# Kernel tuning notes

Hardware: AMD Instinct MI355X
Metric: run time of the kernel (lower is better)

## Reference

```python
import jax, jax.numpy as jnp
import numpy as np
from jax import lax

DIM = 8        # per-head dim
HEADS = 32     # inp // dim
EPS = 1e-15    # linear-attention eps
BN_EPS = 1e-5  # torch BatchNorm2d default eps


def _conv(x, w, groups=1, pad=0):
    return lax.conv_general_dilated(
        x, w, window_strides=(1, 1), padding=[(pad, pad), (pad, pad)],
        feature_group_count=groups,
        dimension_numbers=('NCHW', 'OIHW', 'NCHW'))


def setup_inputs() -> dict:
    key = jax.random.key(0)
    ks = jax.random.split(key, 9)
    B, C, H, W = 8, 256, 64, 64
    td = HEADS * DIM  # 256
    x = jax.random.normal(ks[0], (B, C, H, W), jnp.float32)
    w_qkv = jax.random.normal(ks[1], (3 * td, C, 1, 1), jnp.float32) * 0.05
    w_dw = jax.random.normal(ks[2], (3 * td, 1, 5, 5), jnp.float32) * 0.05
    w_pw = jax.random.normal(ks[3], (3 * td, (3 * td) // (3 * HEADS), 1, 1), jnp.float32) * 0.05
    w_proj = jax.random.normal(ks[4], (C, 2 * td, 1, 1), jnp.float32) * 0.05
    bn_gamma = 1.0 + 0.1 * jax.random.normal(ks[5], (C,), jnp.float32)
    bn_beta = 0.1 * jax.random.normal(ks[6], (C,), jnp.float32)
    bn_mean = 0.1 * jax.random.normal(ks[7], (C,), jnp.float32)
    bn_var = jnp.ones((C,), jnp.float32)
    return dict(x=x, w_qkv=w_qkv, w_dw=w_dw, w_pw=w_pw, w_proj=w_proj,
                bn_gamma=bn_gamma, bn_beta=bn_beta, bn_mean=bn_mean, bn_var=bn_var)


def reference(x, w_qkv, w_dw, w_pw, w_proj, bn_gamma, bn_beta, bn_mean, bn_var):
    B, _, H, W = x.shape
    # qkv: 1x1 conv, no bias/norm/act
    qkv = _conv(x, w_qkv)                                   # (B, 3*td, H, W)
    # aggreg branch: depthwise 5x5 then grouped 1x1 (groups = 3*heads)
    agg = _conv(qkv, w_dw, groups=w_dw.shape[0], pad=2)
    agg = _conv(agg, w_pw, groups=3 * HEADS)
    ms = jnp.concatenate([qkv, agg], axis=1)                # (B, 2*3*td, H, W)
    # relu linear attention
    G = ms.shape[1] // (3 * DIM)                            # 2*heads = 64
    t = ms.reshape(B, G, 3 * DIM, H * W).transpose(0, 1, 3, 2)  # (B, G, N, 3d)
    q = jax.nn.relu(t[..., :DIM])
    k = jax.nn.relu(t[..., DIM:2 * DIM])
    v = t[..., 2 * DIM:]
    v = jnp.pad(v, ((0, 0), (0, 0), (0, 0), (0, 1)), constant_values=1.0)  # ones trick
    kv = jnp.einsum('bgnd,bgne->bgde', k, v)                # (B, G, d, d+1)
    out = jnp.einsum('bgnd,bgde->bgne', q, kv)              # (B, G, N, d+1)
    out = out[..., :-1] / (out[..., -1:] + EPS)
    out = out.transpose(0, 1, 3, 2).reshape(B, G * DIM, H, W)  # (B, 2*td, H, W)
    # proj: 1x1 conv + BatchNorm2d (eval mode), no act
    out = _conv(out, w_proj)
    inv = jax.lax.rsqrt(bn_var + BN_EPS)
    out = (out - bn_mean[:, None, None]) * (inv * bn_gamma)[:, None, None] + bn_beta[:, None, None]
    return out
```

## Files before the change

### kernel.cpp

```cpp
#include <hip/hip_runtime.h>

typedef __bf16 bf16;
typedef __bf16 bf16x4 __attribute__((ext_vector_type(4)));
typedef __bf16 bf16x8 __attribute__((ext_vector_type(8)));
typedef float f32x4 __attribute__((ext_vector_type(4)));

#define NPIX 4096

__global__ __launch_bounds__(256) void split_x(
    const float* __restrict__ x,
    bf16* __restrict__ xTh, bf16* __restrict__ xTm, bf16* __restrict__ xTl)
{
    const int pix = blockIdx.x * 256 + threadIdx.x;
    const int k0  = blockIdx.y * 32;
    const int b   = blockIdx.z;

    const float* __restrict__ src = x + ((size_t)b * 256 + k0) * NPIX + pix;
    float v[32];
#pragma unroll
    for (int kk = 0; kk < 32; ++kk) v[kk] = src[(size_t)kk * NPIX];

    const size_t drow = ((size_t)b * NPIX + pix) * 256 + k0;
#pragma unroll
    for (int c = 0; c < 4; ++c) {
        bf16x8 vh, vm, vl;
#pragma unroll
        for (int j = 0; j < 8; ++j) {
            float val = v[c * 8 + j];
            bf16 h = (bf16)val; float r  = val - (float)h;
            bf16 m = (bf16)r;   float r2 = r - (float)m;
            vh[j] = h; vm[j] = m; vl[j] = (bf16)r2;
        }
        *(bf16x8*)(xTh + drow + c * 8) = vh;
        *(bf16x8*)(xTm + drow + c * 8) = vm;
        *(bf16x8*)(xTl + drow + c * 8) = vl;
    }
}

__global__ __launch_bounds__(256, 2) void qkv_mfma(
    const float* __restrict__ A,
    const bf16* __restrict__ xTh,
    const bf16* __restrict__ xTm,
    const bf16* __restrict__ xTl,
    float* __restrict__ C)
{
    __shared__ bf16 As[3][128][40];

    const int tid  = threadIdx.x;
    const int lane = tid & 63;
    const int wv   = tid >> 6;
    const int col  = lane & 15;
    const int quad = lane >> 4;
    const int wm   = (wv >> 1) * 64;
    const int wn   = (wv & 1) * 64;
    const int n0   = blockIdx.x * 128;
    const int m0   = blockIdx.y * 128;
    const int b    = blockIdx.z;

    const int arow = tid >> 1;
    const int akc  = (tid & 1) * 16;

    const size_t xoff = ((size_t)b * NPIX + n0 + wn) * 256;

    f32x4 acc[4][4] = {};

    float av[16];
    {
        const float* ap = A + (size_t)(m0 + arow) * 256 + akc;
        *(float4*)&av[0]  = *(const float4*)(ap);
        *(float4*)&av[4]  = *(const float4*)(ap + 4);
        *(float4*)&av[8]  = *(const float4*)(ap + 8);
        *(float4*)&av[12] = *(const float4*)(ap + 12);
    }

    for (int k0 = 0; k0 < 256; k0 += 32) {
        __syncthreads();

#pragma unroll
        for (int c = 0; c < 4; ++c) {
            bf16x4 vh, vm, vl;
#pragma unroll
            for (int j = 0; j < 4; ++j) {
                float val = av[c * 4 + j];
                bf16 h = (bf16)val; float r  = val - (float)h;
                bf16 m = (bf16)r;   float r2 = r - (float)m;
                vh[j] = h; vm[j] = m; vl[j] = (bf16)r2;
            }
            *(bf16x4*)&As[0][arow][akc + c * 4] = vh;
            *(bf16x4*)&As[1][arow][akc + c * 4] = vm;
            *(bf16x4*)&As[2][arow][akc + c * 4] = vl;
        }

        if (k0 + 32 < 256) {
            const float* ap = A + (size_t)(m0 + arow) * 256 + k0 + 32 + akc;
            *(float4*)&av[0]  = *(const float4*)(ap);
            *(float4*)&av[4]  = *(const float4*)(ap + 4);
            *(float4*)&av[8]  = *(const float4*)(ap + 8);
            *(float4*)&av[12] = *(const float4*)(ap + 12);
        }

        __syncthreads();

        bf16x8 bh[4], bm[4], bl[4];
#pragma unroll
        for (int t = 0; t < 4; ++t) {
            const size_t brow = xoff + (size_t)(t * 16 + col) * 256 + k0 + quad * 8;
            bh[t] = *(const bf16x8*)(xTh + brow);
            bm[t] = *(const bf16x8*)(xTm + brow);
            bl[t] = *(const bf16x8*)(xTl + brow);
        }
        bf16x8 af[4][3];
#pragma unroll
        for (int s = 0; s < 4; ++s)
#pragma unroll
            for (int p = 0; p < 3; ++p)
                af[s][p] = *(const bf16x8*)&As[p][wm + s * 16 + col][quad * 8];

#pragma unroll
        for (int t = 0; t < 4; ++t)
#pragma unroll
            for (int s = 0; s < 4; ++s)
                acc[s][t] = __builtin_amdgcn_mfma_f32_16x16x32_bf16(af[s][2], bh[t], acc[s][t], 0, 0, 0);
#pragma unroll
        for (int t = 0; t < 4; ++t)
#pragma unroll
            for (int s = 0; s < 4; ++s)
                acc[s][t] = __builtin_amdgcn_mfma_f32_16x16x32_bf16(af[s][0], bl[t], acc[s][t], 0, 0, 0);
#pragma unroll
        for (int t = 0; t < 4; ++t)
#pragma unroll
            for (int s = 0; s < 4; ++s)
                acc[s][t] = __builtin_amdgcn_mfma_f32_16x16x32_bf16(af[s][1], bm[t], acc[s][t], 0, 0, 0);
#pragma unroll
        for (int t = 0; t < 4; ++t)
#pragma unroll
            for (int s = 0; s < 4; ++s)
                acc[s][t] = __builtin_amdgcn_mfma_f32_16x16x32_bf16(af[s][1], bh[t], acc[s][t], 0, 0, 0);
#pragma unroll
        for (int t = 0; t < 4; ++t)
#pragma unroll
            for (int s = 0; s < 4; ++s)
                acc[s][t] = __builtin_amdgcn_mfma_f32_16x16x32_bf16(af[s][0], bm[t], acc[s][t], 0, 0, 0);
#pragma unroll
        for (int t = 0; t < 4; ++t)
#pragma unroll
            for (int s = 0; s < 4; ++s)
                acc[s][t] = __builtin_amdgcn_mfma_f32_16x16x32_bf16(af[s][0], bh[t], acc[s][t], 0, 0, 0);
    }

    float* __restrict__ Cp = C + (size_t)b * 768 * NPIX;
#pragma unroll
    for (int s = 0; s < 4; ++s)
#pragma unroll
        for (int t = 0; t < 4; ++t)
#pragma unroll
            for (int r = 0; r < 4; ++r) {
                const int m = m0 + wm + s * 16 + quad * 4 + r;
                const int n = n0 + wn + t * 16 + col;
                Cp[(size_t)m * NPIX + n] = acc[s][t][r];
            }
}

__global__ __launch_bounds__(256) void dwpw(
    const float* __restrict__ qkv,
    const float* __restrict__ w_dw,
    const float* __restrict__ w_pw,
    float* __restrict__ agg)
{
    __shared__ float sm[8][20][72];

    const int tid = threadIdx.x;
    const int y0  = blockIdx.x * 16;
    const int p   = blockIdx.y;
    const int b   = blockIdx.z;

    const float* __restrict__ src = qkv + ((size_t)b * 768 + 8 * p) * NPIX;

#pragma unroll
    for (int it = 0; it < 10; ++it) {
        int idx = tid + it * 256;
        int c  = idx / 320;
        int r  = idx % 320;
        int sy = r >> 4;
        int x4 = (r & 15) * 4;
        int gy = y0 + sy - 2;
        float4 v = {0.f, 0.f, 0.f, 0.f};
        if ((unsigned)gy < 64u)
            v = *(const float4*)(src + (size_t)c * NPIX + gy * 64 + x4);
        *(float4*)&sm[c][sy][4 + x4] = v;
    }
    if (tid < 160) {
        int c = tid / 20, sy = tid % 20;
        sm[c][sy][2] = 0.f; sm[c][sy][3] = 0.f;
        sm[c][sy][68] = 0.f; sm[c][sy][69] = 0.f;
    }
    __syncthreads();

    const int ty = tid >> 4;
    const int x0 = (tid & 15) * 4;

    float d[8][4];
#pragma unroll
    for (int c = 0; c < 8; ++c) {
        float a0 = 0.f, a1 = 0.f, a2 = 0.f, a3 = 0.f;
        const float* __restrict__ wc = w_dw + (size_t)(8 * p + c) * 25;
#pragma unroll
        for (int ky = 0; ky < 5; ++ky) {
            float r[12];
            *(float4*)&r[0] = *(const float4*)&sm[c][ty + ky][x0];
            *(float4*)&r[4] = *(const float4*)&sm[c][ty + ky][x0 + 4];
            *(float4*)&r[8] = *(const float4*)&sm[c][ty + ky][x0 + 8];
#pragma unroll
            for (int kx = 0; kx < 5; ++kx) {
                const float wv = wc[ky * 5 + kx];
                a0 = fmaf(wv, r[2 + 0 + kx], a0);
                a1 = fmaf(wv, r[2 + 1 + kx], a1);
                a2 = fmaf(wv, r[2 + 2 + kx], a2);
                a3 = fmaf(wv, r[2 + 3 + kx], a3);
            }
        }
        d[c][0] = a0; d[c][1] = a1; d[c][2] = a2; d[c][3] = a3;
    }

    float* __restrict__ dst = agg + ((size_t)b * 768 + 8 * p) * NPIX + (y0 + ty) * 64 + x0;
#pragma unroll
    for (int o = 0; o < 8; ++o) {
        const float* __restrict__ wo = w_pw + (size_t)(8 * p + o) * 8;
        float4 s = {0.f, 0.f, 0.f, 0.f};
#pragma unroll
        for (int i = 0; i < 8; ++i) {
            const float wv = wo[i];
            s.x = fmaf(wv, d[i][0], s.x);
            s.y = fmaf(wv, d[i][1], s.y);
            s.z = fmaf(wv, d[i][2], s.z);
            s.w = fmaf(wv, d[i][3], s.w);
        }
        *(float4*)(dst + (size_t)o * NPIX) = s;
    }
}

__global__ __launch_bounds__(256) void kv_reduce(
    const float* __restrict__ qkv, const float* __restrict__ agg,
    float* __restrict__ kvb)
{
    const int g = blockIdx.x, b = blockIdx.y;
    const float* __restrict__ src = (g < 32) ? qkv : agg;
    const float* __restrict__ base = src + ((size_t)b * 768 + 24 * (g & 31)) * NPIX;

    float acc[72];
#pragma unroll
    for (int i = 0; i < 72; ++i) acc[i] = 0.0f;

    for (int i4 = threadIdx.x; i4 < NPIX / 4; i4 += 256) {
        float4 kf[8], vf[8];
#pragma unroll
        for (int d = 0; d < 8; ++d) {
            float4 t = ((const float4*)(base + (size_t)(8 + d) * NPIX))[i4];
            kf[d].x = fmaxf(0.0f, t.x); kf[d].y = fmaxf(0.0f, t.y);
            kf[d].z = fmaxf(0.0f, t.z); kf[d].w = fmaxf(0.0f, t.w);
        }
#pragma unroll
        for (int e = 0; e < 8; ++e)
            vf[e] = ((const float4*)(base + (size_t)(16 + e) * NPIX))[i4];
#pragma unroll
        for (int d = 0; d < 8; ++d) {
#pragma unroll
            for (int e = 0; e < 8; ++e)
                acc[d * 9 + e] += kf[d].x * vf[e].x + kf[d].y * vf[e].y +
                                  kf[d].z * vf[e].z + kf[d].w * vf[e].w;
            acc[d * 9 + 8] += kf[d].x + kf[d].y + kf[d].z + kf[d].w;
        }
    }

    const int lane = threadIdx.x & 63;
    const int wv   = threadIdx.x >> 6;
#pragma unroll
    for (int i = 0; i < 72; ++i) {
        float v = acc[i];
        v += __shfl_xor(v, 32, 64);
        v += __shfl_xor(v, 16, 64);
        v += __shfl_xor(v, 8, 64);
        v += __shfl_xor(v, 4, 64);
        v += __shfl_xor(v, 2, 64);
        v += __shfl_xor(v, 1, 64);
        acc[i] = v;
    }
    __shared__ float red[4][72];
    if (lane == 0) {
#pragma unroll
        for (int i = 0; i < 72; ++i) red[wv][i] = acc[i];
    }
    __syncthreads();
    if (threadIdx.x < 72)
        kvb[((size_t)b * 64 + g) * 72 + threadIdx.x] =
            red[0][threadIdx.x] + red[1][threadIdx.x] +
            red[2][threadIdx.x] + red[3][threadIdx.x];
}

__global__ __launch_bounds__(256) void attn_fused(
    const float* __restrict__ qkv, const float* __restrict__ agg,
    const float* __restrict__ kvb,
    bf16* __restrict__ attTh, bf16* __restrict__ attTm)
{
    const int b   = blockIdx.y;
    const int n0  = blockIdx.x * 32;
    const int tid = threadIdx.x;
    const int p   = tid & 31;
    const int c   = tid >> 5;

    __shared__ float kvs[64 * 72];
    for (int i = tid; i < 64 * 72; i += 256) kvs[i] = kvb[(size_t)b * 64 * 72 + i];
    __syncthreads();

    const int n = n0 + p;
    const size_t orow = ((size_t)b * NPIX + n) * 512;

#pragma unroll
    for (int gi = 0; gi < 8; ++gi) {
        const int g = c * 8 + gi;
        const float* __restrict__ src = (g < 32) ? qkv : agg;
        const float* __restrict__ base = src + ((size_t)b * 768 + 24 * (g & 31)) * NPIX + n;

        float q[8];
#pragma unroll
        for (int d = 0; d < 8; ++d) q[d] = fmaxf(0.0f, base[(size_t)d * NPIX]);

        const float* kv = &kvs[g * 72];
        float den = 1e-15f;
#pragma unroll
        for (int d = 0; d < 8; ++d) den = fmaf(q[d], kv[d * 9 + 8], den);
        float inv = 1.0f / den;
#pragma unroll
        for (int d = 0; d < 8; ++d) q[d] *= inv;

        bf16x8 vh, vm;
#pragma unroll
        for (int e = 0; e < 8; ++e) {
            float o = 0.0f;
#pragma unroll
            for (int d = 0; d < 8; ++d) o = fmaf(q[d], kv[d * 9 + e], o);
            bf16 h = (bf16)o;
            vh[e] = h;
            vm[e] = (bf16)(o - (float)h);
        }
        *(bf16x8*)(attTh + orow + g * 8) = vh;
        *(bf16x8*)(attTm + orow + g * 8) = vm;
    }
}

__global__ __launch_bounds__(256, 2) void proj_mfma(
    const float* __restrict__ A,
    const bf16* __restrict__ Bh,
    const bf16* __restrict__ Bm,
    float* __restrict__ C,
    const float* __restrict__ bn_g, const float* __restrict__ bn_b,
    const float* __restrict__ bn_m, const float* __restrict__ bn_v)
{
    __shared__ bf16 As[2][128][40];

    const int tid  = threadIdx.x;
    const int lane = tid & 63;
    const int wv   = tid >> 6;
    const int col  = lane & 15;
    const int quad = lane >> 4;
    const int wm   = (wv >> 1) * 64;
    const int wn   = (wv & 1) * 64;
    const int n0   = blockIdx.x * 128;
    const int m0   = blockIdx.y * 128;
    const int b    = blockIdx.z;

    const int arow = tid >> 1;
    const int akc  = (tid & 1) * 16;

    const size_t boff = ((size_t)b * NPIX + n0 + wn) * 512;

    f32x4 acc[4][4] = {};

    float av[16];
    {
        const float* ap = A + (size_t)(m0 + arow) * 512 + akc;
        *(float4*)&av[0]  = *(const float4*)(ap);
        *(float4*)&av[4]  = *(const float4*)(ap + 4);
        *(float4*)&av[8]  = *(const float4*)(ap + 8);
        *(float4*)&av[12] = *(const float4*)(ap + 12);
    }

    for (int k0 = 0; k0 < 512; k0 += 32) {
        __syncthreads();

#pragma unroll
        for (int c = 0; c < 4; ++c) {
            bf16x4 vh, vm;
#pragma unroll
            for (int j = 0; j < 4; ++j) {
                float val = av[c * 4 + j];
                bf16 h = (bf16)val;
                vh[j] = h; vm[j] = (bf16)(val - (float)h);
            }
            *(bf16x4*)&As[0][arow][akc + c * 4] = vh;
            *(bf16x4*)&As[1][arow][akc + c * 4] = vm;
        }

        if (k0 + 32 < 512) {
            const float* ap = A + (size_t)(m0 + arow) * 512 + k0 + 32 + akc;
            *(float4*)&av[0]  = *(const float4*)(ap);
            *(float4*)&av[4]  = *(const float4*)(ap + 4);
            *(float4*)&av[8]  = *(const float4*)(ap + 8);
            *(float4*)&av[12] = *(const float4*)(ap + 12);
        }

        __syncthreads();

        bf16x8 bh[4], bm2[4];
#pragma unroll
        for (int t = 0; t < 4; ++t) {
            const size_t brow = boff + (size_t)(t * 16 + col) * 512 + k0 + quad * 8;
            bh[t]  = *(const bf16x8*)(Bh + brow);
            bm2[t] = *(const bf16x8*)(Bm + brow);
        }
        bf16x8 af[4][2];
#pragma unroll
        for (int s = 0; s < 4; ++s) {
            af[s][0] = *(const bf16x8*)&As[0][wm + s * 16 + col][quad * 8];
            af[s][1] = *(const bf16x8*)&As[1][wm + s * 16 + col][quad * 8];
        }

#pragma unroll
        for (int t = 0; t < 4; ++t)
#pragma unroll
            for (int s = 0; s < 4; ++s)
                acc[s][t] = __builtin_amdgcn_mfma_f32_16x16x32_bf16(af[s][1], bh[t], acc[s][t], 0, 0, 0);
#pragma unroll
        for (int t = 0; t < 4; ++t)
#pragma unroll
            for (int s = 0; s < 4; ++s)
                acc[s][t] = __builtin_amdgcn_mfma_f32_16x16x32_bf16(af[s][0], bm2[t], acc[s][t], 0, 0, 0);
#pragma unroll
        for (int t = 0; t < 4; ++t)
#pragma unroll
            for (int s = 0; s < 4; ++s)
                acc[s][t] = __builtin_amdgcn_mfma_f32_16x16x32_bf16(af[s][0], bh[t], acc[s][t], 0, 0, 0);
    }

    float* __restrict__ Cp = C + (size_t)b * 256 * NPIX;
#pragma unroll
    for (int s = 0; s < 4; ++s) {
#pragma unroll
        for (int r = 0; r < 4; ++r) {
            const int m = m0 + wm + s * 16 + quad * 4 + r;
            const float sc  = (1.0f / sqrtf(bn_v[m] + 1e-5f)) * bn_g[m];
            const float off = bn_b[m] - bn_m[m] * sc;
#pragma unroll
            for (int t = 0; t < 4; ++t) {
                const int n = n0 + wn + t * 16 + col;
                Cp[(size_t)m * NPIX + n] = acc[s][t][r] * sc + off;
            }
        }
    }
}

extern "C" void kernel_launch(void* const* d_in, const int* in_sizes, int n_in,
                              void* d_out, int out_size, void* d_ws, size_t ws_size,
                              hipStream_t stream) {
    const float* x      = (const float*)d_in[0];
    const float* w_qkv  = (const float*)d_in[1];
    const float* w_dw   = (const float*)d_in[2];
    const float* w_pw   = (const float*)d_in[3];
    const float* w_proj = (const float*)d_in[4];
    const float* bn_g   = (const float*)d_in[5];
    const float* bn_b   = (const float*)d_in[6];
    const float* bn_m   = (const float*)d_in[7];
    const float* bn_v   = (const float*)d_in[8];
    float* out = (float*)d_out;

    char* ws = (char*)d_ws;
    float* qkv  = (float*)ws;
    float* agg  = (float*)(ws + 100663296ull);
    char*  r3   = ws + 201326592ull;
    bf16*  xTh  = (bf16*)r3;
    bf16*  xTm  = (bf16*)(r3 + 16777216ull);
    bf16*  xTl  = (bf16*)(r3 + 33554432ull);
    bf16*  attTh = (bf16*)r3;
    bf16*  attTm = (bf16*)(r3 + 33554432ull);
    float* kvb  = (float*)d_out;

    split_x<<<dim3(16, 8, 8), dim3(256), 0, stream>>>(x, xTh, xTm, xTl);

    qkv_mfma<<<dim3(32, 6, 8), dim3(256), 0, stream>>>(w_qkv, xTh, xTm, xTl, qkv);

    dwpw<<<dim3(4, 96, 8), dim3(256), 0, stream>>>(qkv, w_dw, w_pw, agg);

    kv_reduce<<<dim3(64, 8), dim3(256), 0, stream>>>(qkv, agg, kvb);

    attn_fused<<<dim3(128, 8), dim3(256), 0, stream>>>(qkv, agg, kvb, attTh, attTm);

    proj_mfma<<<dim3(32, 2, 8), dim3(256), 0, stream>>>(
        w_proj, attTh, attTm, out, bn_g, bn_b, bn_m, bn_v);
}
```

Measured before the change: 431.0 us.

## Pre-split GEMM weights to bf16 and double-buffer A tiles via global_load_lds

Adds small kernels that split the qkv and proj weights into bf16 hi/mid/lo parts once per call, so the GEMM blocks no longer convert fp32 weights in registers on every tile. The A operand is now staged with direct global-to-LDS loads into a double-buffered shared tile, and the next tile's load is issued before the MFMAs run, which drops one barrier per k-step. The change adds two kernel launches and some workspace, and uses unpadded LDS rows that may cause bank conflicts. The vmcnt(0) wait also covers the B register loads.

```diff
diff --git a/kernel.cpp b/kernel.cpp
--- a/kernel.cpp
+++ b/kernel.cpp
@@ -37,14 +37,34 @@
     }
 }
 
+__global__ __launch_bounds__(256) void split_w3(
+    const float* __restrict__ w,
+    bf16* __restrict__ h, bf16* __restrict__ m, bf16* __restrict__ l)
+{
+    const int i = blockIdx.x * 256 + threadIdx.x;
+    const float v = w[i];
+    const bf16 a = (bf16)v;  const float r1 = v - (float)a;
+    const bf16 c = (bf16)r1;
+    h[i] = a; m[i] = c; l[i] = (bf16)(r1 - (float)c);
+}
+
+__global__ __launch_bounds__(256) void split_w2(
+    const float* __restrict__ w, bf16* __restrict__ h, bf16* __restrict__ m)
+{
+    const int i = blockIdx.x * 256 + threadIdx.x;
+    const float v = w[i];
+    const bf16 a = (bf16)v;
+    h[i] = a; m[i] = (bf16)(v - (float)a);
+}
+
 __global__ __launch_bounds__(256, 2) void qkv_mfma(
-    const float* __restrict__ A,
-    const bf16* __restrict__ xTh,
-    const bf16* __restrict__ xTm,
+    const bf16* __restrict__ Ah, const bf16* __restrict__ Am,
+    const bf16* __restrict__ Al,
+    const bf16* __restrict__ xTh, const bf16* __restrict__ xTm,
     const bf16* __restrict__ xTl,
     float* __restrict__ C)
 {
-    __shared__ bf16 As[3][128][40];
+    __shared__ __align__(16) bf16 As[2][3][128][32];
 
     const int tid  = threadIdx.x;
     const int lane = tid & 63;
@@ -57,64 +77,63 @@
     const int m0   = blockIdx.y * 128;
     const int b    = blockIdx.z;
 
-    const int arow = tid >> 1;
-    const int akc  = (tid & 1) * 16;
-
     const size_t xoff = ((size_t)b * NPIX + n0 + wn) * 256;
 
+    const int srow = wv * 16 + (lane >> 2);
+    const int schk = (lane & 3) * 8;
+
+    const bf16* AP[3] = {Ah, Am, Al};
+
+    auto stage = [&](int buf, int kk) {
+#pragma unroll
+        for (int p = 0; p < 3; ++p)
+#pragma unroll
+            for (int hh = 0; hh < 2; ++hh) {
+                const bf16* gp = AP[p] + (size_t)(m0 + hh * 64 + srow) * 256 + kk + schk;
+                __builtin_amdgcn_global_load_lds(
+                    (const __attribute__((address_space(1))) void*)gp,
+                    (__attribute__((address_space(3))) void*)&As[buf][p][hh * 64 + wv * 16][0],
+                    16, 0, 0);
+            }
+    };
+
     f32x4 acc[4][4] = {};
 
-    float av[16];
-    {
-        const float* ap = A + (size_t)(m0 + arow) * 256 + akc;
-        *(float4*)&av[0]  = *(const float4*)(ap);
-        *(float4*)&av[4]  = *(const float4*)(ap + 4);
-        *(float4*)&av[8]  = *(const float4*)(ap + 8);
-        *(float4*)&av[12] = *(const float4*)(ap + 12);
-    }
-
+    stage(0, 0);
+
+#pragma unroll
     for (int k0 = 0; k0 < 256; k0 += 32) {
-        __syncthreads();
-
-#pragma unroll
-        for (int c = 0; c < 4; ++c) {
-            bf16x4 vh, vm, vl;
-#pragma unroll
-            for (int j = 0; j < 4; ++j) {
-                float val = av[c * 4 + j];
-                bf16 h = (bf16)val; float r  = val - (float)h;
-                bf16 m = (bf16)r;   float r2 = r - (float)m;
-                vh[j] = h; vm[j] = m; vl[j] = (bf16)r2;
-            }
-            *(bf16x4*)&As[0][arow][akc + c * 4] = vh;
-            *(bf16x4*)&As[1][arow][akc + c * 4] = vm;
-            *(bf16x4*)&As[2][arow][akc + c * 4] = vl;
-        }
-
-        if (k0 + 32 < 256) {
-            const float* ap = A + (size_t)(m0 + arow) * 256 + k0 + 32 + akc;
-            *(float4*)&av[0]  = *(const float4*)(ap);
-            *(float4*)&av[4]  = *(const float4*)(ap + 4);
-            *(float4*)&av[8]  = *(const float4*)(ap + 8);
-            *(float4*)&av[12] = *(const float4*)(ap + 12);
-        }
-
-        __syncthreads();
-
-        bf16x8 bh[4], bm[4], bl[4];
+        const int cur = (k0 >> 5) & 1;
+
+        asm volatile("s_waitcnt vmcnt(0)" ::: "memory");
+        __builtin_amdgcn_s_barrier();
+        __builtin_amdgcn_sched_barrier(0);
+
+        bf16x8 af[4][3];
+#pragma unroll
+        for (int s = 0; s < 4; ++s)
+#pragma unroll
+            for (int p = 0; p < 3; ++p)
+                af[s][p] = *(const bf16x8*)&As[cur][p][wm + s * 16 + col][quad * 8];
+
+        if (k0 + 32 < 256) stage(cur ^ 1, k0 + 32);
+
+        bf16x8 bh[4], bl[4], bm[4];
 #pragma unroll
         for (int t = 0; t < 4; ++t) {
             const size_t brow = xoff + (size_t)(t * 16 + col) * 256 + k0 + quad * 8;
             bh[t] = *(const bf16x8*)(xTh + brow);
+        }
+#pragma unroll
+        for (int t = 0; t < 4; ++t) {
+            const size_t brow = xoff + (size_t)(t * 16 + col) * 256 + k0 + quad * 8;
+            bl[t] = *(const bf16x8*)(xTl + brow);
+        }
+#pragma unroll
+        for (int t = 0; t < 4; ++t) {
+            const size_t brow = xoff + (size_t)(t * 16 + col) * 256 + k0 + quad * 8;
             bm[t] = *(const bf16x8*)(xTm + brow);
-            bl[t] = *(const bf16x8*)(xTl + brow);
-        }
-        bf16x8 af[4][3];
-#pragma unroll
-        for (int s = 0; s < 4; ++s)
-#pragma unroll
-            for (int p = 0; p < 3; ++p)
-                af[s][p] = *(const bf16x8*)&As[p][wm + s * 16 + col][quad * 8];
+        }
 
 #pragma unroll
         for (int t = 0; t < 4; ++t)
@@ -349,14 +368,13 @@
 }
 
 __global__ __launch_bounds__(256, 2) void proj_mfma(
-    const float* __restrict__ A,
-    const bf16* __restrict__ Bh,
-    const bf16* __restrict__ Bm,
+    const bf16* __restrict__ Ph, const bf16* __restrict__ Pm,
+    const bf16* __restrict__ Bh, const bf16* __restrict__ Bm,
     float* __restrict__ C,
     const float* __restrict__ bn_g, const float* __restrict__ bn_b,
     const float* __restrict__ bn_m, const float* __restrict__ bn_v)
 {
-    __shared__ bf16 As[2][128][40];
+    __shared__ __align__(16) bf16 As[2][2][128][32];
 
     const int tid  = threadIdx.x;
     const int lane = tid & 63;
@@ -369,77 +387,74 @@
     const int m0   = blockIdx.y * 128;
     const int b    = blockIdx.z;
 
-    const int arow = tid >> 1;
-    const int akc  = (tid & 1) * 16;
-
     const size_t boff = ((size_t)b * NPIX + n0 + wn) * 512;
 
+    const int srow = wv * 16 + (lane >> 2);
+    const int schk = (lane & 3) * 8;
+
+    const bf16* AP[2] = {Ph, Pm};
+
+    auto stage = [&](int buf, int kk) {
+#pragma unroll
+        for (int p = 0; p < 2; ++p)
+#pragma unroll
+            for (int hh = 0; hh < 2; ++hh) {
+                const bf16* gp = AP[p] + (size_t)(m0 + hh * 64 + srow) * 512 + kk + schk;
+                __builtin_amdgcn_global_load_lds(
+                    (const __attribute__((address_space(1))) void*)gp,
+                    (__attribute__((address_space(3))) void*)&As[buf][p][hh * 64 + wv * 16][0],
+                    16, 0, 0);
+            }
+    };
+
     f32x4 acc[4][4] = {};
 
-    float av[16];
-    {
-        const float* ap = A + (size_t)(m0 + arow) * 512 + akc;
-        *(float4*)&av[0]  = *(const float4*)(ap);
-        *(float4*)&av[4]  = *(const float4*)(ap + 4);
-        *(float4*)&av[8]  = *(const float4*)(ap + 8);
-        *(float4*)&av[12] = *(const float4*)(ap + 12);
-    }
-
+    stage(0, 0);
+
+#pragma unroll
     for (int k0 = 0; k0 < 512; k0 += 32) {
-        __syncthreads();
-
-#pragma unroll
-        for (int c = 0; c < 4; ++c) {
-            bf16x4 vh, vm;
-#pragma unroll
-            for (int j = 0; j < 4; ++j) {
-                float val = av[c * 4 + j];
-                bf16 h = (bf16)val;
-                vh[j] = h; vm[j] = (bf16)(val - (float)h);
-            }
-            *(bf16x4*)&As[0][arow][akc + c * 4] = vh;
-            *(bf16x4*)&As[1][arow][akc + c * 4] = vm;
-        }
-
-        if (k0 + 32 < 512) {
-            const float* ap = A + (size_t)(m0 + arow) * 512 + k0 + 32 + akc;
-            *(float4*)&av[0]  = *(const float4*)(ap);
-            *(float4*)&av[4]  = *(const float4*)(ap + 4);
-            *(float4*)&av[8]  = *(const float4*)(ap + 8);
-            *(float4*)&av[12] = *(const float4*)(ap + 12);
-        }
-
-        __syncthreads();
+        const int cur = (k0 >> 5) & 1;
+
+        asm volatile("s_waitcnt vmcnt(0)" ::: "memory");
+        __builtin_amdgcn_s_barrier();
+        __builtin_amdgcn_sched_barrier(0);
+
+        bf16x8 af0[4], af1[4];
+#pragma unroll
+        for (int s = 0; s < 4; ++s) {
+            af0[s] = *(const bf16x8*)&As[cur][0][wm + s * 16 + col][quad * 8];
+            af1[s] = *(const bf16x8*)&As[cur][1][wm + s * 16 + col][quad * 8];
+        }
+
+        if (k0 + 32 < 512) stage(cur ^ 1, k0 + 32);
 
         bf16x8 bh[4], bm2[4];
 #pragma unroll
         for (int t = 0; t < 4; ++t) {
             const size_t brow = boff + (size_t)(t * 16 + col) * 512 + k0 + quad * 8;
-            bh[t]  = *(const bf16x8*)(Bh + brow);
+            bh[t] = *(const bf16x8*)(Bh + brow);
+        }
+#pragma unroll
+        for (int t = 0; t < 4; ++t) {
+            const size_t brow = boff + (size_t)(t * 16 + col) * 512 + k0 + quad * 8;
             bm2[t] = *(const bf16x8*)(Bm + brow);
         }
-        bf16x8 af[4][2];
-#pragma unroll
-        for (int s = 0; s < 4; ++s) {
-            af[s][0] = *(const bf16x8*)&As[0][wm + s * 16 + col][quad * 8];
-            af[s][1] = *(const bf16x8*)&As[1][wm + s * 16 + col][quad * 8];
-        }
-
-#pragma unroll
-        for (int t = 0; t < 4; ++t)
-#pragma unroll
-            for (int s = 0; s < 4; ++s)
-                acc[s][t] = __builtin_amdgcn_mfma_f32_16x16x32_bf16(af[s][1], bh[t], acc[s][t], 0, 0, 0);
-#pragma unroll
-        for (int t = 0; t < 4; ++t)
-#pragma unroll
-            for (int s = 0; s < 4; ++s)
-                acc[s][t] = __builtin_amdgcn_mfma_f32_16x16x32_bf16(af[s][0], bm2[t], acc[s][t], 0, 0, 0);
-#pragma unroll
-        for (int t = 0; t < 4; ++t)
-#pragma unroll
-            for (int s = 0; s < 4; ++s)
-                acc[s][t] = __builtin_amdgcn_mfma_f32_16x16x32_bf16(af[s][0], bh[t], acc[s][t], 0, 0, 0);
+
+#pragma unroll
+        for (int t = 0; t < 4; ++t)
+#pragma unroll
+            for (int s = 0; s < 4; ++s)
+                acc[s][t] = __builtin_amdgcn_mfma_f32_16x16x32_bf16(af1[s], bh[t], acc[s][t], 0, 0, 0);
+#pragma unroll
+        for (int t = 0; t < 4; ++t)
+#pragma unroll
+            for (int s = 0; s < 4; ++s)
+                acc[s][t] = __builtin_amdgcn_mfma_f32_16x16x32_bf16(af0[s], bm2[t], acc[s][t], 0, 0, 0);
+#pragma unroll
+        for (int t = 0; t < 4; ++t)
+#pragma unroll
+            for (int s = 0; s < 4; ++s)
+                acc[s][t] = __builtin_amdgcn_mfma_f32_16x16x32_bf16(af0[s], bh[t], acc[s][t], 0, 0, 0);
     }
 
     float* __restrict__ Cp = C + (size_t)b * 256 * NPIX;
@@ -480,13 +495,21 @@
     bf16*  xTh  = (bf16*)r3;
     bf16*  xTm  = (bf16*)(r3 + 16777216ull);
     bf16*  xTl  = (bf16*)(r3 + 33554432ull);
+    bf16*  wqh  = (bf16*)(r3 + 50331648ull);
+    bf16*  wqm  = (bf16*)(r3 + 50331648ull + 393216ull);
+    bf16*  wql  = (bf16*)(r3 + 50331648ull + 786432ull);
     bf16*  attTh = (bf16*)r3;
     bf16*  attTm = (bf16*)(r3 + 33554432ull);
+    bf16*  wph  = (bf16*)ws;
+    bf16*  wpm  = (bf16*)(ws + 262144ull);
     float* kvb  = (float*)d_out;
 
     split_x<<<dim3(16, 8, 8), dim3(256), 0, stream>>>(x, xTh, xTm, xTl);
 
-    qkv_mfma<<<dim3(32, 6, 8), dim3(256), 0, stream>>>(w_qkv, xTh, xTm, xTl, qkv);
+    split_w3<<<dim3(768), dim3(256), 0, stream>>>(w_qkv, wqh, wqm, wql);
+
+    qkv_mfma<<<dim3(32, 6, 8), dim3(256), 0, stream>>>(
+        wqh, wqm, wql, xTh, xTm, xTl, qkv);
 
     dwpw<<<dim3(4, 96, 8), dim3(256), 0, stream>>>(qkv, w_dw, w_pw, agg);
 
@@ -494,6 +517,8 @@
 
     attn_fused<<<dim3(128, 8), dim3(256), 0, stream>>>(qkv, agg, kvb, attTh, attTm);
 
+    split_w2<<<dim3(512), dim3(256), 0, stream>>>(w_proj, wph, wpm);
+
     proj_mfma<<<dim3(32, 2, 8), dim3(256), 0, stream>>>(
-        w_proj, attTh, attTm, out, bn_g, bn_b, bn_m, bn_v);
-}
+        wph, wpm, attTh, attTm, out, bn_g, bn_b, bn_m, bn_v);
+}
```

Measured after the change: 419.2 us. 2.7% less time.
